# Performance work log

Measured on AMD Instinct MI355X. Metric: run time of the kernel, lower is better.

Reference implementation:

```python
import jax, jax.numpy as jnp
import numpy as np

DIM = 384
HEADS = 12
WS = 7
HID = 4 * 256  # FFN hidden is hard-coded default 1024, NOT 4*dim
EPS = 1e-5


def layernorm(x, g, b):
    mu = jnp.mean(x, axis=-1, keepdims=True)
    var = jnp.mean(jnp.square(x - mu), axis=-1, keepdims=True)
    return (x - mu) * jax.lax.rsqrt(var + EPS) * g + b


def setup_inputs() -> dict:
    key = jax.random.key(0)
    ks = jax.random.split(key, 12)
    s = 0.02
    return {
        "x": jax.random.normal(ks[0], (32, DIM, 56, 56), dtype=jnp.float32),
        "ln1_g": jnp.ones((DIM,), jnp.float32),
        "ln1_b": jnp.zeros((DIM,), jnp.float32),
        "qkv_w": jax.random.normal(ks[1], (3 * DIM, DIM), jnp.float32) * s,
        "qkv_b": jnp.zeros((3 * DIM,), jnp.float32),
        "proj_w": jax.random.normal(ks[2], (DIM, DIM), jnp.float32) * s,
        "proj_b": jnp.zeros((DIM,), jnp.float32),
        "ln2_g": jnp.ones((DIM,), jnp.float32),
        "ln2_b": jnp.zeros((DIM,), jnp.float32),
        "fc1_w": jax.random.normal(ks[3], (HID, DIM), jnp.float32) * s,
        "fc1_b": jnp.zeros((HID,), jnp.float32),
        "fc2_w": jax.random.normal(ks[4], (DIM, HID), jnp.float32) * s,
        "fc2_b": jnp.zeros((DIM,), jnp.float32),
    }


def window_attention(x, qkv_w, qkv_b, proj_w, proj_b):
    # x: [B, H, W, C] channels-last
    B, H, W, C = x.shape
    Wh, Ww = H // WS, W // WS
    # partition: [B*Wh*Ww, WS*WS, C]
    w = x.reshape(B, Wh, WS, Ww, WS, C).transpose(0, 1, 3, 2, 4, 5)
    w = w.reshape(B * Wh * Ww, WS * WS, C)
    Bn, N, _ = w.shape
    hd = C // HEADS
    qkv = w @ qkv_w.T + qkv_b  # [Bn, N, 3C]
    qkv = qkv.reshape(Bn, N, 3, HEADS, hd).transpose(2, 0, 3, 1, 4)
    q, k, v = qkv[0], qkv[1], qkv[2]  # each [Bn, h, N, hd]
    attn = jnp.einsum('bhnd,bhmd->bhnm', q, k) * (hd ** -0.5)
    attn = jax.nn.softmax(attn, axis=-1)
    o = jnp.einsum('bhnm,bhmd->bhnd', attn, v)
    o = o.transpose(0, 2, 1, 3).reshape(Bn, N, C)
    o = o @ proj_w.T + proj_b
    # reverse
    o = o.reshape(B, Wh, Ww, WS, WS, C).transpose(0, 1, 3, 2, 4, 5)
    return o.reshape(B, H, W, C)


def reference(x, ln1_g, ln1_b, qkv_w, qkv_b, proj_w, proj_b,
              ln2_g, ln2_b, fc1_w, fc1_b, fc2_w, fc2_b):
    # x: [B, C, H, W]
    residual = x
    h = x.transpose(0, 2, 3, 1)  # [B,H,W,C]
    h = layernorm(h, ln1_g, ln1_b)
    h = window_attention(h, qkv_w, qkv_b, proj_w, proj_b)
    x = h.transpose(0, 3, 1, 2) + residual
    residual = x
    h = x.transpose(0, 2, 3, 1)
    h = layernorm(h, ln2_g, ln2_b)
    h = jax.nn.gelu(h @ fc1_w.T + fc1_b, approximate=False)
    h = h @ fc2_w.T + fc2_b
    return h.transpose(0, 3, 1, 2) + residual
```

## Files before the change

kernel.cpp:

```cpp
#include <hip/hip_runtime.h>
#include <cstdint>
#include <cmath>

#define DIM 384
#define HEADS 12
#define TOKENS 100352
#define HW_ 3136
#define NWIN 2048

typedef __attribute__((ext_vector_type(8))) short short8;
typedef __attribute__((ext_vector_type(4))) short short4v;
typedef __attribute__((ext_vector_type(2))) short short2v;
typedef __attribute__((ext_vector_type(4))) float f32x4;

#define AS1 __attribute__((address_space(1)))
#define AS3 __attribute__((address_space(3)))

__device__ __forceinline__ short f2b(float f){
  unsigned u = __builtin_bit_cast(unsigned, f);
  u += 0x7FFFu + ((u >> 16) & 1u);
  return (short)(u >> 16);
}
__device__ __forceinline__ float b2f(short h){
  unsigned u = ((unsigned)(unsigned short)h) << 16;
  return __builtin_bit_cast(float, u);
}

__device__ __forceinline__ void gload_lds16(const short* g, short* l){
  __builtin_amdgcn_global_load_lds((AS1 void*)(g), (AS3 void*)(l), 16, 0, 0);
}

__device__ __forceinline__ float gelu_f(float v){
  float z  = v * 0.70710678118654752f;
  float az = fabsf(z);
  float t  = __builtin_amdgcn_rcpf(1.f + 0.3275911f*az);
  float poly = t*(0.254829592f + t*(-0.284496736f + t*(1.421413741f +
               t*(-1.453152027f + t*1.061405429f))));
  float e  = __expf(-z*z);
  float er = copysignf(1.f - poly*e, z);
  return 0.5f * v * (1.f + er);
}

__global__ void k_cvt(const float* __restrict__ s, short* __restrict__ d, int n){
  int i = blockIdx.x*256 + threadIdx.x;
  if (i < n) d[i] = f2b(s[i]);
}

__global__ __launch_bounds__(256) void k_ln1(const float* __restrict__ x,
    const float* __restrict__ gam, const float* __restrict__ bet,
    short* __restrict__ ln1, short* __restrict__ xr)
{
  __shared__ float red0[256];
  __shared__ float red1[256];
  __shared__ float mus[64], rss[64];
  __shared__ short lnc[64*36];
  __shared__ short xc[64*36];
  int t = threadIdx.x;
  int blk = blockIdx.x;
  int b = blk / 49;
  int hw0 = (blk % 49) * 64;
  int p = t & 63, cq = t >> 6;
  const float* xb = x + (long)b*DIM*HW_ + hw0 + p;
  float s = 0.f, sq = 0.f;
  for (int i = 0; i < 96; i++){
    int c = i*4 + cq;
    float v = xb[(long)c*HW_];
    s += v; sq += v*v;
  }
  red0[t] = s; red1[t] = sq;
  __syncthreads();
  if (t < 64){
    float ts = red0[t] + red0[t+64] + red0[t+128] + red0[t+192];
    float tq = red1[t] + red1[t+64] + red1[t+128] + red1[t+192];
    float mu = ts * (1.f/DIM);
    float var = tq * (1.f/DIM) - mu*mu;
    mus[t] = mu;
    rss[t] = rsqrtf(var + 1e-5f);
  }
  __syncthreads();
  float mu_p = mus[p], rs_p = rss[p];
  int p2 = t >> 2, q4 = t & 3;
  int hwp2 = hw0 + p2;
  int h2 = hwp2 / 56, w2 = hwp2 % 56;
  int wt2 = ((b*8 + h2/7)*8 + w2/7)*49 + (h2%7)*7 + (w2%7);
  long lnbase = (long)wt2*DIM;
  long xrbase = (long)(b*HW_ + hwp2)*DIM;
  for (int cc0 = 0; cc0 < DIM; cc0 += 32){
    #pragma unroll
    for (int u = 0; u < 8; u++){
      int c = cc0 + cq*8 + u;
      float v = xb[(long)c*HW_];
      float nv = (v - mu_p)*rs_p*gam[c] + bet[c];
      lnc[p*36 + cq*8 + u] = f2b(nv);
      xc[p*36 + cq*8 + u] = f2b(v);
    }
    __syncthreads();
    short8 av, bv;
    #pragma unroll
    for (int u = 0; u < 8; u++){
      av[u] = lnc[p2*36 + q4*8 + u];
      bv[u] = xc[p2*36 + q4*8 + u];
    }
    *(short8*)(ln1 + lnbase + cc0 + q4*8) = av;
    *(short8*)(xr + xrbase + cc0 + q4*8) = bv;
    __syncthreads();
  }
}

#define EPI_BIAS 0
#define EPI_PROJ 1
#define EPI_GELU 2
#define EPI_OUT  4

template<int EPI>
__global__ __launch_bounds__(256) void k_gemm(
    const short* __restrict__ A, const short* __restrict__ B,
    const float* __restrict__ bias, short* __restrict__ out,
    const short* __restrict__ res, int M, int N, int K, int ntiles)
{
  constexpr int ES = (EPI == EPI_OUT) ? 133 : 132;
  __shared__ short sm[20480];
  float* E = (float*)sm;

  int nwg = gridDim.x;
  int orig = blockIdx.x;
  int bid = (orig & 7) * (nwg >> 3) + (orig >> 3);
  int nt = bid % ntiles, mt = bid / ntiles;
  int m0 = mt*128, n0 = nt*128;
  int t = threadIdx.x;
  int lane = t & 63, wv = t >> 6;
  int wm = wv >> 1, wn = wv & 1;
  int gg = lane >> 4, cc = lane & 15;

  int srow = t >> 2;
  int skc = ((t & 3) ^ (srow & 3)) << 3;
  const short* Ab = A + (long)(m0 + srow)*K + skc;
  const short* Bb = B + (long)(n0 + srow)*K + skc;
  long rowstep = 64L*K;

  int goff = (gg << 3) ^ ((cc & 3) << 3);

  f32x4 acc[4][4];
  #pragma unroll
  for (int i=0;i<4;i++)
    #pragma unroll
    for (int j=0;j<4;j++) acc[i][j] = (f32x4){0.f,0.f,0.f,0.f};

  int nk = K >> 5;

  gload_lds16(Ab,           sm + t*8);
  gload_lds16(Ab + rowstep, sm + (t+256)*8);
  gload_lds16(Bb,           sm + 12288 + t*8);
  gload_lds16(Bb + rowstep, sm + 12288 + (t+256)*8);
  gload_lds16(Ab + 32,           sm + 4096 + t*8);
  gload_lds16(Ab + 32 + rowstep, sm + 4096 + (t+256)*8);

  int ac = 0, bc = 0;
  for (int kt = 0; kt < nk; kt++){
    if (kt + 1 < nk) { asm volatile("s_waitcnt vmcnt(2) lgkmcnt(0)" ::: "memory"); }
    else             { asm volatile("s_waitcnt vmcnt(0) lgkmcnt(0)" ::: "memory"); }
    __builtin_amdgcn_s_barrier();
    if (kt + 1 < nk){
      long ko = (long)(kt+1) << 5;
      int bn = bc ^ 1;
      gload_lds16(Bb + ko,           sm + 12288 + bn*4096 + t*8);
      gload_lds16(Bb + ko + rowstep, sm + 12288 + bn*4096 + (t+256)*8);
    }
    if (kt + 2 < nk){
      long ko = (long)(kt+2) << 5;
      int an = ac + 2; if (an >= 3) an -= 3;
      gload_lds16(Ab + ko,           sm + an*4096 + t*8);
      gload_lds16(Ab + ko + rowstep, sm + an*4096 + (t+256)*8);
    }
    const short* Ac = sm + ac*4096;
    const short* Bc = sm + 12288 + bc*4096;
    short8 af[4], bfv[4];
    #pragma unroll
    for (int mi=0;mi<4;mi++) af[mi] = *(const short8*)(Ac + (wm*64 + mi*16 + cc)*32 + goff);
    #pragma unroll
    for (int ni=0;ni<4;ni++) bfv[ni] = *(const short8*)(Bc + (wn*64 + ni*16 + cc)*32 + goff);
    #pragma unroll
    for (int mi=0;mi<4;mi++)
      #pragma unroll
      for (int ni=0;ni<4;ni++)
        acc[mi][ni] = __builtin_amdgcn_mfma_f32_16x16x32_bf16(af[mi], bfv[ni], acc[mi][ni], 0, 0, 0);
    ac = (ac + 1 == 3) ? 0 : ac + 1;
    bc ^= 1;
  }

  if constexpr (EPI == EPI_OUT) {
    float* outf = (float*)out;
    #pragma unroll
    for (int p = 0; p < 2; p++){
      __syncthreads();
      if (wm == p){
        #pragma unroll
        for (int mi=0;mi<4;mi++){
          #pragma unroll
          for (int r=0;r<4;r++){
            float* Er = E + (mi*16 + gg*4 + r)*ES + wn*64 + cc;
            Er[0]  = acc[mi][0][r];
            Er[16] = acc[mi][1][r];
            Er[32] = acc[mi][2][r];
            Er[48] = acc[mi][3][r];
          }
        }
      }
      __syncthreads();
      #pragma unroll
      for (int jj = 0; jj < 8; jj++){
        int unit = jj*256 + t;
        int crow = unit >> 5, chunk = unit & 31;
        int row = m0 + p*64 + crow;
        f32x4 v = *(const f32x4*)(E + crow*ES + chunk*4);
        f32x4 bv = *(const f32x4*)(bias + n0 + chunk*4);
        short4v rv = *(const short4v*)(res + (long)row*N + n0 + chunk*4);
        #pragma unroll
        for (int j = 0; j < 4; j++) v[j] += bv[j] + b2f(rv[j]);
        *(f32x4*)(E + crow*ES + chunk*4) = v;
      }
      __syncthreads();
      #pragma unroll
      for (int jj = 0; jj < 32; jj++){
        int unit = jj*256 + t;
        int c = unit >> 6, rl = unit & 63;
        int token = m0 + p*64 + rl;
        int b = token / HW_;
        int hw = token - b*HW_;
        outf[((long)b*DIM + n0 + c)*HW_ + hw] = E[rl*ES + c];
      }
    }
  } else {
    #pragma unroll
    for (int p = 0; p < 2; p++){
      __syncthreads();
      #pragma unroll
      for (int mh = 0; mh < 2; mh++){
        #pragma unroll
        for (int r = 0; r < 4; r++){
          int crow = wm*32 + mh*16 + gg*4 + r;
          float* Er = E + crow*ES + wn*64 + cc;
          Er[0]  = acc[mh*2 + p][0][r];
          Er[16] = acc[mh*2 + p][1][r];
          Er[32] = acc[mh*2 + p][2][r];
          Er[48] = acc[mh*2 + p][3][r];
        }
      }
      __syncthreads();
      #pragma unroll
      for (int jj = 0; jj < 8; jj++){
        int unit = jj*256 + t;
        int crow = unit >> 5, chunk = unit & 31;
        int rr = crow & 15, mh = (crow >> 4) & 1, wmr = crow >> 5;
        int row = m0 + wmr*64 + (mh*2 + p)*16 + rr;
        int col = n0 + chunk*4;
        f32x4 v = *(const f32x4*)(E + crow*ES + chunk*4);
        f32x4 bv = *(const f32x4*)(bias + col);
        long orow;
        if constexpr (EPI == EPI_PROJ) {
          int b = row / HW_; int rem = row % HW_;
          int wid = rem / 49, idx = rem % 49;
          int hh = (wid >> 3)*7 + idx/7;
          int ww = (wid & 7)*7 + idx%7;
          orow = (long)(b*HW_ + hh*56 + ww)*N;
        } else {
          orow = (long)row*N;
        }
        float vv[4];
        #pragma unroll
        for (int j = 0; j < 4; j++){
          vv[j] = v[j] + bv[j];
          if constexpr (EPI == EPI_GELU) vv[j] = gelu_f(vv[j]);
        }
        if constexpr (EPI == EPI_PROJ){
          short4v rv = *(const short4v*)(res + orow + col);
          #pragma unroll
          for (int j = 0; j < 4; j++) vv[j] += b2f(rv[j]);
        }
        short4v ov;
        #pragma unroll
        for (int j = 0; j < 4; j++) ov[j] = f2b(vv[j]);
        *(short4v*)(out + orow + col) = ov;
      }
    }
  }
}

__global__ __launch_bounds__(256) void k_ln2(const short* __restrict__ x2,
  const float* __restrict__ gam, const float* __restrict__ bet, short* __restrict__ o)
{
  int t = threadIdx.x, lane = t & 63, wv = t >> 6;
  long row = (long)blockIdx.x*4 + wv;
  const short* xr = x2 + row*DIM;
  short4v a = *(const short4v*)(xr + lane*4);
  short2v b2 = *(const short2v*)(xr + 256 + lane*2);
  float f[6] = {b2f(a[0]),b2f(a[1]),b2f(a[2]),b2f(a[3]),b2f(b2[0]),b2f(b2[1])};
  float s = 0.f, sq = 0.f;
  #pragma unroll
  for (int i=0;i<6;i++){ s += f[i]; sq += f[i]*f[i]; }
  #pragma unroll
  for (int off=1; off<64; off<<=1){ s += __shfl_xor(s, off); sq += __shfl_xor(sq, off); }
  float mu = s*(1.f/DIM);
  float var = sq*(1.f/DIM) - mu*mu;
  float rs = rsqrtf(var + 1e-5f);
  int c0 = lane*4, c1 = 256 + lane*2;
  short4v oa; short2v ob;
  #pragma unroll
  for (int i=0;i<4;i++) oa[i] = f2b((f[i]-mu)*rs*gam[c0+i] + bet[c0+i]);
  #pragma unroll
  for (int j=0;j<2;j++) ob[j] = f2b((f[4+j]-mu)*rs*gam[c1+j] + bet[c1+j]);
  *(short4v*)(o + row*DIM + c0) = oa;
  *(short2v*)(o + row*DIM + c1) = ob;
}

__global__ __launch_bounds__(256) void k_attn(const short* __restrict__ qkv, short* __restrict__ o)
{
  __shared__ short lds[4*7424];
  int t = threadIdx.x;
  int lane = t & 63, wv = t >> 6;
  int w = blockIdx.x;
  short* Qs = lds + wv*7424;
  short* Ks = Qs + 2560;
  short* Vt = Ks + 2560;
  short* Pl = Qs;
  int g = lane >> 4, c = lane & 15;
  int nrow = lane >> 2;
  int dc = (lane & 3) * 8;
  const float scale = 0.17677669529663687f;
  for (int hh = 0; hh < 3; hh++){
    int h = wv + hh*4;
    __syncthreads();
    long base = (long)w*49*1152 + h*32;
    #pragma unroll
    for (int it = 0; it < 4; it++){
      int n = it*16 + nrow;
      short8 vq = {0,0,0,0,0,0,0,0};
      short8 vk = vq, vvv = vq;
      if (n < 49){
        vq  = *(const short8*)(qkv + base + (long)n*1152 + dc);
        vk  = *(const short8*)(qkv + base + (long)n*1152 + 384 + dc);
        vvv = *(const short8*)(qkv + base + (long)n*1152 + 768 + dc);
      }
      *(short8*)(Qs + n*40 + dc) = vq;
      *(short8*)(Ks + n*40 + dc) = vk;
      #pragma unroll
      for (int u = 0; u < 8; u++) Vt[(dc+u)*72 + n] = vvv[u];
    }
    __syncthreads();
    f32x4 sacc[4][4];
    #pragma unroll
    for (int i=0;i<4;i++)
      #pragma unroll
      for (int j=0;j<4;j++) sacc[i][j] = (f32x4){0.f,0.f,0.f,0.f};
    short8 kf[4];
    #pragma unroll
    for (int ni=0;ni<4;ni++) kf[ni] = *(const short8*)(Ks + (ni*16 + c)*40 + g*8);
    #pragma unroll
    for (int mi=0;mi<4;mi++){
      short8 a = *(const short8*)(Qs + (mi*16 + c)*40 + g*8);
      #pragma unroll
      for (int ni=0;ni<4;ni++)
        sacc[mi][ni] = __builtin_amdgcn_mfma_f32_16x16x32_bf16(a, kf[ni], sacc[mi][ni], 0, 0, 0);
    }
    #pragma unroll
    for (int mi=0;mi<4;mi++){
      #pragma unroll
      for (int r=0;r<4;r++){
        float v0 = sacc[mi][0][r]*scale;
        float v1 = sacc[mi][1][r]*scale;
        float v2 = sacc[mi][2][r]*scale;
        float v3 = (c >= 1) ? -1e30f : sacc[mi][3][r]*scale;
        float mx = fmaxf(fmaxf(v0,v1), fmaxf(v2,v3));
        #pragma unroll
        for (int off=1; off<16; off<<=1) mx = fmaxf(mx, __shfl_xor(mx, off));
        float e0 = __expf(v0-mx), e1 = __expf(v1-mx), e2 = __expf(v2-mx), e3 = __expf(v3-mx);
        float sm = e0+e1+e2+e3;
        #pragma unroll
        for (int off=1; off<16; off<<=1) sm += __shfl_xor(sm, off);
        float inv = 1.f/sm;
        int prow = mi*16 + g*4 + r;
        Pl[prow*72 +      c] = f2b(e0*inv);
        Pl[prow*72 + 16 + c] = f2b(e1*inv);
        Pl[prow*72 + 32 + c] = f2b(e2*inv);
        Pl[prow*72 + 48 + c] = f2b(e3*inv);
      }
    }
    __syncthreads();
    f32x4 oacc[4][2];
    #pragma unroll
    for (int i=0;i<4;i++){ oacc[i][0] = (f32x4){0.f,0.f,0.f,0.f}; oacc[i][1] = oacc[i][0]; }
    #pragma unroll
    for (int ks=0; ks<2; ks++){
      short8 bb0 = *(const short8*)(Vt + (c)*72      + ks*32 + g*8);
      short8 bb1 = *(const short8*)(Vt + (16 + c)*72 + ks*32 + g*8);
      #pragma unroll
      for (int mi=0;mi<4;mi++){
        short8 aa = *(const short8*)(Pl + (mi*16 + c)*72 + ks*32 + g*8);
        oacc[mi][0] = __builtin_amdgcn_mfma_f32_16x16x32_bf16(aa, bb0, oacc[mi][0], 0, 0, 0);
        oacc[mi][1] = __builtin_amdgcn_mfma_f32_16x16x32_bf16(aa, bb1, oacc[mi][1], 0, 0, 0);
      }
    }
    #pragma unroll
    for (int mi=0;mi<4;mi++){
      #pragma unroll
      for (int r=0;r<4;r++){
        int row = mi*16 + g*4 + r;
        if (row < 49){
          long ob = ((long)w*49 + row)*384 + h*32;
          o[ob + c]      = f2b(oacc[mi][0][r]);
          o[ob + 16 + c] = f2b(oacc[mi][1][r]);
        }
      }
    }
  }
}

extern "C" void kernel_launch(void* const* d_in, const int* in_sizes, int n_in,
                              void* d_out, int out_size, void* d_ws, size_t ws_size,
                              hipStream_t stream) {
  (void)in_sizes; (void)n_in; (void)out_size; (void)ws_size;
  const float* x      = (const float*)d_in[0];
  const float* ln1_g  = (const float*)d_in[1];
  const float* ln1_b  = (const float*)d_in[2];
  const float* qkv_w  = (const float*)d_in[3];
  const float* qkv_b  = (const float*)d_in[4];
  const float* proj_w = (const float*)d_in[5];
  const float* proj_b = (const float*)d_in[6];
  const float* ln2_g  = (const float*)d_in[7];
  const float* ln2_b  = (const float*)d_in[8];
  const float* fc1_w  = (const float*)d_in[9];
  const float* fc1_b  = (const float*)d_in[10];
  const float* fc2_w  = (const float*)d_in[11];
  const float* fc2_b  = (const float*)d_in[12];

  char* ws = (char*)d_ws;
  short* buf1 = (short*)(ws);
  short* buf2 = (short*)(ws + 231211008L);
  short* buf3 = (short*)(ws + 308281344L);
  short* buf4 = (short*)(ws + 385351680L);
  short* buf5 = (short*)(ws + 462422016L);
  short* wq = (short*)(ws + 539492352L);
  short* wp = wq + 442368;
  short* w1 = wp + 147456;
  short* w2 = w1 + 393216;

  k_cvt<<<dim3((442368+255)/256), dim3(256), 0, stream>>>(qkv_w, wq, 442368);
  k_cvt<<<dim3((147456+255)/256), dim3(256), 0, stream>>>(proj_w, wp, 147456);
  k_cvt<<<dim3((393216+255)/256), dim3(256), 0, stream>>>(fc1_w, w1, 393216);
  k_cvt<<<dim3((393216+255)/256), dim3(256), 0, stream>>>(fc2_w, w2, 393216);

  k_ln1<<<dim3(1568), dim3(256), 0, stream>>>(x, ln1_g, ln1_b, buf2, buf5);

  k_gemm<EPI_BIAS><<<dim3(784*9), dim3(256), 0, stream>>>(buf2, wq, qkv_b, buf1, nullptr,
                                                          TOKENS, 1152, 384, 9);
  k_attn<<<dim3(NWIN), dim3(256), 0, stream>>>(buf1, buf3);

  k_gemm<EPI_PROJ><<<dim3(784*3), dim3(256), 0, stream>>>(buf3, wp, proj_b, buf4, buf5,
                                                          TOKENS, 384, 384, 3);
  k_ln2<<<dim3(TOKENS/4), dim3(256), 0, stream>>>(buf4, ln2_g, ln2_b, buf2);

  k_gemm<EPI_GELU><<<dim3(784*8), dim3(256), 0, stream>>>(buf2, w1, fc1_b, buf1, nullptr,
                                                          TOKENS, 1024, 384, 8);
  k_gemm<EPI_OUT><<<dim3(784*3), dim3(256), 0, stream>>>(buf1, w2, fc2_b, (short*)d_out, buf4,
                                                         TOKENS, 384, 1024, 3);
}
```

Baseline: 760.1 us.

## Split attention heads across grid and cache x in LDS for LN1

The attention kernel now launches a 3x larger grid so each block handles one head per wave, and block-wide barriers are replaced with wave-local LDS waits. This removes the serial loop over head groups and the __syncthreads stalls. LN1 reads x from global memory once, keeps it as bf16 in a full LDS tile, and computes the normalization from that bf16 copy. This drops the second strided pass over x but slightly changes precision and increases LDS use.

```diff
diff --git a/kernel.cpp b/kernel.cpp
--- a/kernel.cpp
+++ b/kernel.cpp
@@ -53,8 +53,7 @@
   __shared__ float red0[256];
   __shared__ float red1[256];
   __shared__ float mus[64], rss[64];
-  __shared__ short lnc[64*36];
-  __shared__ short xc[64*36];
+  __shared__ short xfull[64*388];
   int t = threadIdx.x;
   int blk = blockIdx.x;
   int b = blk / 49;
@@ -66,6 +65,7 @@
     int c = i*4 + cq;
     float v = xb[(long)c*HW_];
     s += v; sq += v*v;
+    xfull[p*388 + c] = f2b(v);
   }
   red0[t] = s; red1[t] = sq;
   __syncthreads();
@@ -78,32 +78,25 @@
     rss[t] = rsqrtf(var + 1e-5f);
   }
   __syncthreads();
-  float mu_p = mus[p], rs_p = rss[p];
   int p2 = t >> 2, q4 = t & 3;
+  float mu = mus[p2], rs = rss[p2];
   int hwp2 = hw0 + p2;
   int h2 = hwp2 / 56, w2 = hwp2 % 56;
   int wt2 = ((b*8 + h2/7)*8 + w2/7)*49 + (h2%7)*7 + (w2%7);
   long lnbase = (long)wt2*DIM;
   long xrbase = (long)(b*HW_ + hwp2)*DIM;
+  #pragma unroll
   for (int cc0 = 0; cc0 < DIM; cc0 += 32){
+    short8 xv = *(const short8*)(xfull + p2*388 + cc0 + q4*8);
+    short8 lv;
     #pragma unroll
     for (int u = 0; u < 8; u++){
-      int c = cc0 + cq*8 + u;
-      float v = xb[(long)c*HW_];
-      float nv = (v - mu_p)*rs_p*gam[c] + bet[c];
-      lnc[p*36 + cq*8 + u] = f2b(nv);
-      xc[p*36 + cq*8 + u] = f2b(v);
-    }
-    __syncthreads();
-    short8 av, bv;
-    #pragma unroll
-    for (int u = 0; u < 8; u++){
-      av[u] = lnc[p2*36 + q4*8 + u];
-      bv[u] = xc[p2*36 + q4*8 + u];
-    }
-    *(short8*)(ln1 + lnbase + cc0 + q4*8) = av;
-    *(short8*)(xr + xrbase + cc0 + q4*8) = bv;
-    __syncthreads();
+      int c = cc0 + q4*8 + u;
+      float v = b2f(xv[u]);
+      lv[u] = f2b((v - mu)*rs*gam[c] + bet[c]);
+    }
+    *(short8*)(ln1 + lnbase + cc0 + q4*8) = lv;
+    *(short8*)(xr + xrbase + cc0 + q4*8) = xv;
   }
 }
 
@@ -319,6 +312,7 @@
   int t = threadIdx.x;
   int lane = t & 63, wv = t >> 6;
   int w = blockIdx.x;
+  int h = wv + (int)blockIdx.y*4;
   short* Qs = lds + wv*7424;
   short* Ks = Qs + 2560;
   short* Vt = Ks + 2560;
@@ -327,89 +321,90 @@
   int nrow = lane >> 2;
   int dc = (lane & 3) * 8;
   const float scale = 0.17677669529663687f;
-  for (int hh = 0; hh < 3; hh++){
-    int h = wv + hh*4;
-    __syncthreads();
-    long base = (long)w*49*1152 + h*32;
-    #pragma unroll
-    for (int it = 0; it < 4; it++){
-      int n = it*16 + nrow;
-      short8 vq = {0,0,0,0,0,0,0,0};
-      short8 vk = vq, vvv = vq;
-      if (n < 49){
-        vq  = *(const short8*)(qkv + base + (long)n*1152 + dc);
-        vk  = *(const short8*)(qkv + base + (long)n*1152 + 384 + dc);
-        vvv = *(const short8*)(qkv + base + (long)n*1152 + 768 + dc);
-      }
-      *(short8*)(Qs + n*40 + dc) = vq;
-      *(short8*)(Ks + n*40 + dc) = vk;
-      #pragma unroll
-      for (int u = 0; u < 8; u++) Vt[(dc+u)*72 + n] = vvv[u];
-    }
-    __syncthreads();
-    f32x4 sacc[4][4];
-    #pragma unroll
-    for (int i=0;i<4;i++)
-      #pragma unroll
-      for (int j=0;j<4;j++) sacc[i][j] = (f32x4){0.f,0.f,0.f,0.f};
-    short8 kf[4];
-    #pragma unroll
-    for (int ni=0;ni<4;ni++) kf[ni] = *(const short8*)(Ks + (ni*16 + c)*40 + g*8);
+
+  long base = (long)w*49*1152 + h*32;
+  #pragma unroll
+  for (int it = 0; it < 4; it++){
+    int n = it*16 + nrow;
+    short8 vq = {0,0,0,0,0,0,0,0};
+    short8 vk = vq, vvv = vq;
+    if (n < 49){
+      vq  = *(const short8*)(qkv + base + (long)n*1152 + dc);
+      vk  = *(const short8*)(qkv + base + (long)n*1152 + 384 + dc);
+      vvv = *(const short8*)(qkv + base + (long)n*1152 + 768 + dc);
+    }
+    *(short8*)(Qs + n*40 + dc) = vq;
+    *(short8*)(Ks + n*40 + dc) = vk;
+    #pragma unroll
+    for (int u = 0; u < 8; u++) Vt[(dc+u)*72 + n] = vvv[u];
+  }
+  asm volatile("s_waitcnt lgkmcnt(0)" ::: "memory");
+  __builtin_amdgcn_sched_barrier(0);
+
+  f32x4 sacc[4][4];
+  #pragma unroll
+  for (int i=0;i<4;i++)
+    #pragma unroll
+    for (int j=0;j<4;j++) sacc[i][j] = (f32x4){0.f,0.f,0.f,0.f};
+  short8 kf[4];
+  #pragma unroll
+  for (int ni=0;ni<4;ni++) kf[ni] = *(const short8*)(Ks + (ni*16 + c)*40 + g*8);
+  #pragma unroll
+  for (int mi=0;mi<4;mi++){
+    short8 a = *(const short8*)(Qs + (mi*16 + c)*40 + g*8);
+    #pragma unroll
+    for (int ni=0;ni<4;ni++)
+      sacc[mi][ni] = __builtin_amdgcn_mfma_f32_16x16x32_bf16(a, kf[ni], sacc[mi][ni], 0, 0, 0);
+  }
+  #pragma unroll
+  for (int mi=0;mi<4;mi++){
+    #pragma unroll
+    for (int r=0;r<4;r++){
+      float v0 = sacc[mi][0][r]*scale;
+      float v1 = sacc[mi][1][r]*scale;
+      float v2 = sacc[mi][2][r]*scale;
+      float v3 = (c >= 1) ? -1e30f : sacc[mi][3][r]*scale;
+      float mx = fmaxf(fmaxf(v0,v1), fmaxf(v2,v3));
+      #pragma unroll
+      for (int off=1; off<16; off<<=1) mx = fmaxf(mx, __shfl_xor(mx, off));
+      float e0 = __expf(v0-mx), e1 = __expf(v1-mx), e2 = __expf(v2-mx), e3 = __expf(v3-mx);
+      float sm = e0+e1+e2+e3;
+      #pragma unroll
+      for (int off=1; off<16; off<<=1) sm += __shfl_xor(sm, off);
+      float inv = 1.f/sm;
+      int prow = mi*16 + g*4 + r;
+      Pl[prow*72 +      c] = f2b(e0*inv);
+      Pl[prow*72 + 16 + c] = f2b(e1*inv);
+      Pl[prow*72 + 32 + c] = f2b(e2*inv);
+      Pl[prow*72 + 48 + c] = f2b(e3*inv);
+    }
+  }
+  asm volatile("s_waitcnt lgkmcnt(0)" ::: "memory");
+  __builtin_amdgcn_sched_barrier(0);
+
+  f32x4 oacc[4][2];
+  #pragma unroll
+  for (int i=0;i<4;i++){ oacc[i][0] = (f32x4){0.f,0.f,0.f,0.f}; oacc[i][1] = oacc[i][0]; }
+  #pragma unroll
+  for (int ks=0; ks<2; ks++){
+    short8 bb0 = *(const short8*)(Vt + (c)*72      + ks*32 + g*8);
+    short8 bb1 = *(const short8*)(Vt + (16 + c)*72 + ks*32 + g*8);
     #pragma unroll
     for (int mi=0;mi<4;mi++){
-      short8 a = *(const short8*)(Qs + (mi*16 + c)*40 + g*8);
-      #pragma unroll
-      for (int ni=0;ni<4;ni++)
-        sacc[mi][ni] = __builtin_amdgcn_mfma_f32_16x16x32_bf16(a, kf[ni], sacc[mi][ni], 0, 0, 0);
-    }
-    #pragma unroll
-    for (int mi=0;mi<4;mi++){
-      #pragma unroll
-      for (int r=0;r<4;r++){
-        float v0 = sacc[mi][0][r]*scale;
-        float v1 = sacc[mi][1][r]*scale;
-        float v2 = sacc[mi][2][r]*scale;
-        float v3 = (c >= 1) ? -1e30f : sacc[mi][3][r]*scale;
-        float mx = fmaxf(fmaxf(v0,v1), fmaxf(v2,v3));
-        #pragma unroll
-        for (int off=1; off<16; off<<=1) mx = fmaxf(mx, __shfl_xor(mx, off));
-        float e0 = __expf(v0-mx), e1 = __expf(v1-mx), e2 = __expf(v2-mx), e3 = __expf(v3-mx);
-        float sm = e0+e1+e2+e3;
-        #pragma unroll
-        for (int off=1; off<16; off<<=1) sm += __shfl_xor(sm, off);
-        float inv = 1.f/sm;
-        int prow = mi*16 + g*4 + r;
-        Pl[prow*72 +      c] = f2b(e0*inv);
-        Pl[prow*72 + 16 + c] = f2b(e1*inv);
-        Pl[prow*72 + 32 + c] = f2b(e2*inv);
-        Pl[prow*72 + 48 + c] = f2b(e3*inv);
-      }
-    }
-    __syncthreads();
-    f32x4 oacc[4][2];
-    #pragma unroll
-    for (int i=0;i<4;i++){ oacc[i][0] = (f32x4){0.f,0.f,0.f,0.f}; oacc[i][1] = oacc[i][0]; }
-    #pragma unroll
-    for (int ks=0; ks<2; ks++){
-      short8 bb0 = *(const short8*)(Vt + (c)*72      + ks*32 + g*8);
-      short8 bb1 = *(const short8*)(Vt + (16 + c)*72 + ks*32 + g*8);
-      #pragma unroll
-      for (int mi=0;mi<4;mi++){
-        short8 aa = *(const short8*)(Pl + (mi*16 + c)*72 + ks*32 + g*8);
-        oacc[mi][0] = __builtin_amdgcn_mfma_f32_16x16x32_bf16(aa, bb0, oacc[mi][0], 0, 0, 0);
-        oacc[mi][1] = __builtin_amdgcn_mfma_f32_16x16x32_bf16(aa, bb1, oacc[mi][1], 0, 0, 0);
-      }
-    }
-    #pragma unroll
-    for (int mi=0;mi<4;mi++){
-      #pragma unroll
-      for (int r=0;r<4;r++){
-        int row = mi*16 + g*4 + r;
-        if (row < 49){
-          long ob = ((long)w*49 + row)*384 + h*32;
-          o[ob + c]      = f2b(oacc[mi][0][r]);
-          o[ob + 16 + c] = f2b(oacc[mi][1][r]);
-        }
+      short8 aa = *(const short8*)(Pl + (mi*16 + c)*72 + ks*32 + g*8);
+      oacc[mi][0] = __builtin_amdgcn_mfma_f32_16x16x32_bf16(aa, bb0, oacc[mi][0], 0, 0, 0);
+      oacc[mi][1] = __builtin_amdgcn_mfma_f32_16x16x32_bf16(aa, bb1, oacc[mi][1], 0, 0, 0);
+    }
+  }
+  #pragma unroll
+  for (int mi=0;mi<4;mi++){
+    #pragma unroll
+    for (int r=0;r<4;r++){
+      int row = mi*16 + g*4 + r;
+      if (row < 49){
+        long ob = ((long)w*49 + row)*384 + h*32;
+        o[ob + c]      = f2b(oacc[mi][0][r]);
+        o[ob + 16 + c] = f2b(oacc[mi][1][r]);
       }
     }
   }
@@ -453,7 +448,7 @@
 
   k_gemm<EPI_BIAS><<<dim3(784*9), dim3(256), 0, stream>>>(buf2, wq, qkv_b, buf1, nullptr,
                                                           TOKENS, 1152, 384, 9);
-  k_attn<<<dim3(NWIN), dim3(256), 0, stream>>>(buf1, buf3);
+  k_attn<<<dim3(NWIN, 3), dim3(256), 0, stream>>>(buf1, buf3);
 
   k_gemm<EPI_PROJ><<<dim3(784*3), dim3(256), 0, stream>>>(buf3, wp, proj_b, buf4, buf5,
                                                           TOKENS, 384, 384, 3);
```

New measurement: 720.5 us. -5.2%, faster.
